# Kernel tuning notes

Hardware: AMD Instinct MI355X
Metric: run time of the kernel (lower is better)

Reference implementation:

```python
import jax, jax.numpy as jnp
import numpy as np

B, S, H, D = 2, 2048, 16, 64
DM = H * D  # 1024


def setup_inputs() -> dict:
    key = jax.random.key(0)
    ks = jax.random.split(key, 5)
    scale = 0.02
    return {
        "hidden_states": jax.random.normal(ks[0], (B, S, DM), dtype=jnp.float32),
        "Wq": scale * jax.random.normal(ks[1], (DM, DM), dtype=jnp.float32),
        "bq": jnp.zeros((DM,), jnp.float32),
        "Wk": scale * jax.random.normal(ks[2], (DM, DM), dtype=jnp.float32),
        "bk": jnp.zeros((DM,), jnp.float32),
        "Wv": scale * jax.random.normal(ks[3], (DM, DM), dtype=jnp.float32),
        "bv": jnp.zeros((DM,), jnp.float32),
        "Wy": scale * jax.random.normal(ks[4], (DM, DM), dtype=jnp.float32),
        "by": jnp.zeros((DM,), jnp.float32),
    }


def _split_heads(x):
    # [B,S,H*D] -> [B,H,S,D]
    b, s, _ = x.shape
    return x.reshape(b, s, H, D).transpose(0, 2, 1, 3)


def _merge_heads(x):
    # [B,H,S,D] -> [B,S,H*D]
    b, h, s, d = x.shape
    return x.transpose(0, 2, 1, 3).reshape(b, s, h * d)


def reference(hidden_states, Wq, bq, Wk, bk, Wv, bv, Wy, by):
    q = _split_heads(hidden_states @ Wq.T + bq)  # [B,H,S,D]
    k = _split_heads(hidden_states @ Wk.T + bk)
    v = _split_heads(hidden_states @ Wv.T + bv)

    logits = jnp.einsum("bhsd,bhtd->bhst", q, k) / jnp.sqrt(jnp.float32(D))
    mask = jnp.tril(jnp.ones((S, S), jnp.float32))  # causal lower-triangular mask

    # Faithful to the original module's hand-rolled masked softmax:
    # denominator = sum_t exp(logits) * mask ; numerator = exp(logits*mask - 1e4*(1-mask))
    denom = jnp.sum(jnp.exp(logits) * mask, axis=3, keepdims=True)
    numer = jnp.exp(logits * mask - 1e4 * (1.0 - mask))
    weights = numer / denom  # [B,H,S,S]

    attended = jnp.einsum("bhst,bhtd->bhsd", weights, v)
    out = _merge_heads(attended)  # [B,S,H*D]
    return out @ Wy.T + by
```

## Files before the change

kernel.cpp:

```cpp
#include <hip/hip_runtime.h>

#define DEV __device__ __forceinline__

typedef __attribute__((ext_vector_type(8))) short bf16x8;
typedef __attribute__((ext_vector_type(4))) float f32x4;
typedef __attribute__((ext_vector_type(16))) float f32x16;

DEV ushort f2bf(float f) {
  union { float f; unsigned u; } x; x.f = f;
  unsigned r = (x.u + 0x7FFFu + ((x.u >> 16) & 1u)) >> 16;
  return (ushort)r;
}

DEV void gload16(const void* g, void* l) {
  __builtin_amdgcn_global_load_lds(
      (const __attribute__((address_space(1))) void*)g,
      (__attribute__((address_space(3))) void*)l, 16, 0, 0);
}

DEV f32x4 mfma16(bf16x8 a, bf16x8 b, f32x4 c) {
  return __builtin_amdgcn_mfma_f32_16x16x32_bf16(a, b, c, 0, 0, 0);
}
DEV f32x16 mfma32(bf16x8 a, bf16x8 b, f32x16 c) {
  return __builtin_amdgcn_mfma_f32_32x32x16_bf16(a, b, c, 0, 0, 0);
}

DEV unsigned cvtpk(float a, float b) {
  unsigned r;
  asm("v_cvt_pk_bf16_f32 %0, %1, %2" : "=v"(r) : "v"(a), "v"(b));
  return r;
}

#if __has_builtin(__builtin_amdgcn_exp2f)
#define EXP2(x) __builtin_amdgcn_exp2f(x)
#else
#define EXP2(x) exp2f(x)
#endif

#define BB 2
#define SS 2048
#define HH 16
#define DD 64
#define DM 1024
#define MROWS (BB * SS)
#define NQKV  (3 * DM)
#define NQK   (2 * DM)

__global__ void convert_kernel(const float* __restrict__ hs,
                               const float* __restrict__ Wq, const float* __restrict__ bq,
                               const float* __restrict__ Wk, const float* __restrict__ bk,
                               const float* __restrict__ Wv, const float* __restrict__ bv,
                               const float* __restrict__ Wy,
                               ushort* __restrict__ Xb, ushort* __restrict__ Wqkv,
                               ushort* __restrict__ Wyb, float* __restrict__ bqkv) {
  const int HS_V = (MROWS * DM) / 4;
  const int WQ_V = (NQKV * DM) / 4;
  const int WY_V = (DM * DM) / 4;
  int idx = blockIdx.x * 256 + threadIdx.x;
  if (idx < HS_V) {
    float4 v = ((const float4*)hs)[idx];
    ushort4 o; o.x = f2bf(v.x); o.y = f2bf(v.y); o.z = f2bf(v.z); o.w = f2bf(v.w);
    ((ushort4*)Xb)[idx] = o;
  } else if (idx < HS_V + WQ_V) {
    int e = (idx - HS_V) * 4;
    int n = e >> 10, k = e & 1023;
    const float* W = (n < 1024) ? Wq : (n < 2048) ? Wk : Wv;
    int nn = n & 1023;
    float4 v = *(const float4*)(W + nn * 1024 + k);
    ushort4 o; o.x = f2bf(v.x); o.y = f2bf(v.y); o.z = f2bf(v.z); o.w = f2bf(v.w);
    ((ushort4*)Wqkv)[idx - HS_V] = o;
  } else if (idx < HS_V + WQ_V + WY_V) {
    int e = idx - HS_V - WQ_V;
    float4 v = ((const float4*)Wy)[e];
    ushort4 o; o.x = f2bf(v.x); o.y = f2bf(v.y); o.z = f2bf(v.z); o.w = f2bf(v.w);
    ((ushort4*)Wyb)[e] = o;
  }
  if (idx < NQKV)
    bqkv[idx] = (idx < 1024) ? bq[idx] : (idx < 2048) ? bk[idx - 1024] : bv[idx - 2048];
}

template <int BM, bool OUT_F32, bool VSPLIT>
__global__ void gemm_bt(const ushort* __restrict__ A, const ushort* __restrict__ Bw,
                        const float* __restrict__ bias, void* __restrict__ Cout,
                        ushort* __restrict__ VtOut,
                        int M, int N, int K, int Nc, int scaleN, float qscale) {
  constexpr int NI = BM / 32;
  __shared__ ushort Al[BM * 64];
  __shared__ ushort Bl[128 * 64];
  const int tid = threadIdx.x;
  const int lane = tid & 63;
  const int wave = tid >> 6;
  const int lg = lane >> 4, l15 = lane & 15;
  const int m0 = blockIdx.x * BM, n0 = blockIdx.y * 128;
  const int wm = (wave >> 1) * (BM / 2), wn = (wave & 1) * 64;

  f32x4 acc[NI][4] = {};

  for (int k0 = 0; k0 < K; k0 += 64) {
#pragma unroll
    for (int s = 0; s < BM * 8 / 256; ++s) {
      int f = tid + s * 256;
      int row = f >> 3, c = f & 7, cs = c ^ (row & 7);
      gload16(A + (size_t)(m0 + row) * K + k0 + cs * 8, (char*)Al + f * 16);
    }
#pragma unroll
    for (int s = 0; s < 4; ++s) {
      int f = tid + s * 256;
      int row = f >> 3, c = f & 7, cs = c ^ (row & 7);
      gload16(Bw + (size_t)(n0 + row) * K + k0 + cs * 8, (char*)Bl + f * 16);
    }
    __syncthreads();

#pragma unroll
    for (int kk = 0; kk < 2; ++kk) {
      bf16x8 af[NI], bfr[4];
#pragma unroll
      for (int i = 0; i < NI; ++i) {
        int rA = wm + i * 16 + l15;
        int cA = (kk * 4 + lg) ^ (rA & 7);
        af[i] = *(const bf16x8*)((const char*)Al + rA * 128 + cA * 16);
      }
#pragma unroll
      for (int j = 0; j < 4; ++j) {
        int rB = wn + j * 16 + l15;
        int cB = (kk * 4 + lg) ^ (rB & 7);
        bfr[j] = *(const bf16x8*)((const char*)Bl + rB * 128 + cB * 16);
      }
#pragma unroll
      for (int i = 0; i < NI; ++i)
#pragma unroll
        for (int j = 0; j < 4; ++j)
          acc[i][j] = mfma16(af[i], bfr[j], acc[i][j]);
    }
    __syncthreads();
  }

  if (VSPLIT && n0 >= 2048) {
#pragma unroll
    for (int i = 0; i < NI; ++i) {
#pragma unroll
      for (int j = 0; j < 4; ++j) {
        int n = n0 + wn + j * 16 + l15;
        float bv = bias[n];
        int h = (n >> 6) & 15, d = n & 63;
        int mb = m0 + wm + i * 16 + lg * 4;
        int b = mb >> 11, s = mb & 2047;
        ushort4 o;
        o.x = f2bf(acc[i][j][0] + bv);
        o.y = f2bf(acc[i][j][1] + bv);
        o.z = f2bf(acc[i][j][2] + bv);
        o.w = f2bf(acc[i][j][3] + bv);
        *(ushort4*)(VtOut + ((size_t)(b * 16 + h) * 64 + d) * SS + s) = o;
      }
    }
  } else {
#pragma unroll
    for (int i = 0; i < NI; ++i) {
#pragma unroll
      for (int j = 0; j < 4; ++j) {
        int n = n0 + wn + j * 16 + l15;
        float bv = bias[n];
        float qs = (n < scaleN) ? qscale : 1.0f;
#pragma unroll
        for (int r = 0; r < 4; ++r) {
          int m = m0 + wm + i * 16 + lg * 4 + r;
          float v = (acc[i][j][r] + bv) * qs;
          if (OUT_F32)
            ((float*)Cout)[(size_t)m * Nc + n] = v;
          else
            ((ushort*)Cout)[(size_t)m * Nc + n] = f2bf(v);
        }
      }
    }
  }
}

__global__ __launch_bounds__(256, 2)
void attn_kernel(const ushort* __restrict__ QK, const ushort* __restrict__ Vt,
                 ushort* __restrict__ Ob) {
  __shared__ __align__(16) char SMEM[65536];

  const int tid = threadIdx.x;
  const int wave = tid >> 6, lane = tid & 63;
  const int l31 = lane & 31, hi = lane >> 5;
  const int grp = wave >> 1, wq = wave & 1;

  const int n = blockIdx.x;
  const int bh = (n & 7) | ((n >> 7) << 3);
  const int pairi = (n >> 3) & 15;
  const int b = bh >> 4, h = bh & 15;

  int px = lane, pw = 1000;
  asm volatile("v_permlane32_swap_b32 %0, %1" : "+v"(px), "+v"(pw));
  const bool defA = (__builtin_amdgcn_readfirstlane(px) == 0);

  const int gtid = tid & 127;
  const int srow = gtid >> 3;
  const int scs = (gtid & 7) ^ (srow & 7);
  const ushort* Kg = QK + (size_t)(b * SS + srow) * NQK + DM + h * 64 + scs * 8;
  const ushort* Vg = Vt + (size_t)(bh * 64 + srow) * SS + scs * 8;

#define STAGE(d_, kv0_) do {                                            \
    const ushort* kg_ = Kg + (size_t)(kv0_) * NQK;                      \
    const ushort* vg_ = Vg + (kv0_);                                    \
    char* kl_ = SMEM + (grp * 2 + (d_)) * 8192 + gtid * 16;             \
    char* vl_ = SMEM + 32768 + (grp * 2 + (d_)) * 8192 + gtid * 16;     \
    _Pragma("unroll")                                                   \
    for (int s_ = 0; s_ < 4; ++s_) {                                    \
      gload16(kg_ + (size_t)s_ * 16 * NQK, kl_ + s_ * 2048);            \
      gload16(vg_ + (size_t)s_ * 16 * SS,  vl_ + s_ * 2048);            \
    }                                                                   \
  } while (0)

  union U4 { unsigned u[4]; bf16x8 v; };

#define PACKH(sv, R, D0, D1, D2, D3) do {                              \
    unsigned X = cvtpk(sv[R + 0], sv[R + 1]);                          \
    unsigned Y = cvtpk(sv[R + 2], sv[R + 3]);                          \
    unsigned W = cvtpk(sv[R + 4], sv[R + 5]);                          \
    unsigned Z = cvtpk(sv[R + 6], sv[R + 7]);                          \
    if (defA) {                                                        \
      asm volatile("v_permlane32_swap_b32 %0, %1" : "+v"(X), "+v"(W)); \
      asm volatile("v_permlane32_swap_b32 %0, %1" : "+v"(Y), "+v"(Z)); \
    } else {                                                           \
      asm volatile("v_permlane32_swap_b32 %0, %1" : "+v"(W), "+v"(X)); \
      asm volatile("v_permlane32_swap_b32 %0, %1" : "+v"(Z), "+v"(Y)); \
    }                                                                  \
    D0 = X; D1 = Y; D2 = W; D3 = Z;                                    \
  } while (0)

#pragma unroll 1
  for (int ph = 0; ph < 2; ++ph) {
    __builtin_amdgcn_s_barrier();

    const int qt = ph ? (31 - pairi) : pairi;
    const int q0 = qt * 64;
    const int nkv = qt + 1;
    const int niter = (nkv + 1) >> 1;
    const int qw = q0 + wq * 32;
    const int q_lane = qw + l31;

    const ushort* Qrow = QK + (size_t)(b * SS + q_lane) * NQK + h * 64 + hi * 8;
    bf16x8 qf0 = *(const bf16x8*)(Qrow);
    bf16x8 qf1 = *(const bf16x8*)(Qrow + 16);
    bf16x8 qf2 = *(const bf16x8*)(Qrow + 32);
    bf16x8 qf3 = *(const bf16x8*)(Qrow + 48);

    f32x16 acc0 = {}, acc1 = {};
    float ps0 = 0.f, ps1 = 0.f, ps2 = 0.f, ps3 = 0.f;

    if (grp < nkv) STAGE(0, grp * 64);
    int buf = 0;

#pragma unroll 1
    for (int it = 0; it < niter; ++it) {
      const int j = 2 * it + grp;
      if (j + 2 < nkv) {
        STAGE(buf ^ 1, (j + 2) * 64);
        asm volatile("s_waitcnt vmcnt(8)" ::: "memory");
      } else {
        asm volatile("s_waitcnt vmcnt(0)" ::: "memory");
      }
      __builtin_amdgcn_s_barrier();
      __builtin_amdgcn_sched_barrier(0);

      if (j < nkv) {
        const int kv0 = j * 64;
        const char* Kb = SMEM + (grp * 2 + buf) * 8192;
        const char* Vb = SMEM + 32768 + (grp * 2 + buf) * 8192;

        f32x16 s0 = {}, s1 = {};
        __builtin_amdgcn_s_setprio(1);
#pragma unroll
        for (int ks = 0; ks < 4; ++ks) {
          const int ch = (((ks * 2 + hi) ^ (l31 & 7)) * 16);
          bf16x8 kfa = *(const bf16x8*)(Kb + l31 * 128 + ch);
          bf16x8 kfb = *(const bf16x8*)(Kb + (l31 + 32) * 128 + ch);
          bf16x8 qk = (ks == 0) ? qf0 : (ks == 1) ? qf1 : (ks == 2) ? qf2 : qf3;
          s0 = mfma32(kfa, qk, s0);
          s1 = mfma32(kfb, qk, s1);
        }
        __builtin_amdgcn_s_setprio(0);

        if (j == qt) {
#pragma unroll
          for (int r = 0; r < 16; ++r) {
            const int tb = (r & 3) + 8 * (r >> 2) + 4 * hi;
            if (kv0 + tb > q_lane) s0[r] = -1e30f;
            if (kv0 + 32 + tb > q_lane) s1[r] = -1e30f;
          }
        }

#pragma unroll
        for (int r = 0; r < 16; r += 4) {
          float a0 = EXP2(s0[r]), a1 = EXP2(s0[r + 1]), a2 = EXP2(s0[r + 2]), a3 = EXP2(s0[r + 3]);
          s0[r] = a0; s0[r + 1] = a1; s0[r + 2] = a2; s0[r + 3] = a3;
          ps0 += a0; ps1 += a1; ps2 += a2; ps3 += a3;
          float b0 = EXP2(s1[r]), b1 = EXP2(s1[r + 1]), b2 = EXP2(s1[r + 2]), b3 = EXP2(s1[r + 3]);
          s1[r] = b0; s1[r + 1] = b1; s1[r + 2] = b2; s1[r + 3] = b3;
          ps0 += b0; ps1 += b1; ps2 += b2; ps3 += b3;
        }

        U4 f0, f1, f2, f3;
        PACKH(s0, 0, f0.u[0], f0.u[1], f0.u[2], f0.u[3]);
        PACKH(s0, 8, f1.u[0], f1.u[1], f1.u[2], f1.u[3]);
        PACKH(s1, 0, f2.u[0], f2.u[1], f2.u[2], f2.u[3]);
        PACKH(s1, 8, f3.u[0], f3.u[1], f3.u[2], f3.u[3]);

        __builtin_amdgcn_s_setprio(1);
#pragma unroll
        for (int ts = 0; ts < 4; ++ts) {
          const int ch = (((ts * 2 + hi) ^ (l31 & 7)) * 16);
          bf16x8 vfa = *(const bf16x8*)(Vb + l31 * 128 + ch);
          bf16x8 vfb = *(const bf16x8*)(Vb + (l31 + 32) * 128 + ch);
          bf16x8 pf = (ts == 0) ? f0.v : (ts == 1) ? f1.v : (ts == 2) ? f2.v : f3.v;
          acc0 = mfma32(vfa, pf, acc0);
          acc1 = mfma32(vfb, pf, acc1);
        }
        __builtin_amdgcn_s_setprio(0);
      }
      __builtin_amdgcn_sched_barrier(0);
      __builtin_amdgcn_s_barrier();
      buf ^= 1;
    }

    float psum = ps0 + ps1 + ps2 + ps3;
    f32x4* MA = (f32x4*)SMEM;
    float* MP = (float*)(SMEM + 32768);
    const int slot = wq * 64 + lane;
    if (grp == 1) {
#pragma unroll
      for (int c = 0; c < 4; ++c) {
        f32x4 t0 = {acc0[4 * c], acc0[4 * c + 1], acc0[4 * c + 2], acc0[4 * c + 3]};
        MA[c * 128 + slot] = t0;
        f32x4 t1 = {acc1[4 * c], acc1[4 * c + 1], acc1[4 * c + 2], acc1[4 * c + 3]};
        MA[(c + 4) * 128 + slot] = t1;
      }
      MP[slot] = psum;
    }
    __builtin_amdgcn_s_barrier();
    if (grp == 0) {
#pragma unroll
      for (int c = 0; c < 4; ++c) {
        f32x4 t0 = MA[c * 128 + slot];
        f32x4 t1 = MA[(c + 4) * 128 + slot];
        acc0[4 * c] += t0[0]; acc0[4 * c + 1] += t0[1];
        acc0[4 * c + 2] += t0[2]; acc0[4 * c + 3] += t0[3];
        acc1[4 * c] += t1[0]; acc1[4 * c + 1] += t1[1];
        acc1[4 * c + 2] += t1[2]; acc1[4 * c + 3] += t1[3];
      }
      psum += MP[slot];
      float tot = psum + __shfl_xor(psum, 32, 64);
      float inv = 1.0f / tot;
      ushort* orow = Ob + (size_t)(b * SS + q_lane) * DM + h * 64;
#pragma unroll
      for (int g = 0; g < 4; ++g) {
        uint2 st;
        st.x = cvtpk(acc0[4 * g + 0] * inv, acc0[4 * g + 1] * inv);
        st.y = cvtpk(acc0[4 * g + 2] * inv, acc0[4 * g + 3] * inv);
        *(uint2*)(orow + 8 * g + 4 * hi) = st;
        uint2 st2;
        st2.x = cvtpk(acc1[4 * g + 0] * inv, acc1[4 * g + 1] * inv);
        st2.y = cvtpk(acc1[4 * g + 2] * inv, acc1[4 * g + 3] * inv);
        *(uint2*)(orow + 32 + 8 * g + 4 * hi) = st2;
      }
    }
  }
#undef STAGE
#undef PACKH
}

extern "C" void kernel_launch(void* const* d_in, const int* in_sizes, int n_in,
                              void* d_out, int out_size, void* d_ws, size_t ws_size,
                              hipStream_t stream) {
  const float* hs = (const float*)d_in[0];
  const float* Wq = (const float*)d_in[1];
  const float* bq = (const float*)d_in[2];
  const float* Wk = (const float*)d_in[3];
  const float* bk = (const float*)d_in[4];
  const float* Wv = (const float*)d_in[5];
  const float* bv = (const float*)d_in[6];
  const float* Wy = (const float*)d_in[7];
  const float* by = (const float*)d_in[8];
  float* out = (float*)d_out;

  char* ws = (char*)d_ws;
  ushort* Xb   = (ushort*)(ws);
  ushort* Wqkv = (ushort*)(ws + (8ull  << 20));
  ushort* Wyb  = (ushort*)(ws + (14ull << 20));
  float*  bqkv = (float*) (ws + (16ull << 20));
  ushort* QK   = (ushort*)(ws + (17ull << 20));
  ushort* Vt   = (ushort*)(ws + (33ull << 20));
  ushort* Ob   = (ushort*)(ws + (41ull << 20));

  const float QSC = 0.125f * 1.44269504088896f;

  convert_kernel<<<dim3(8192), dim3(256), 0, stream>>>(hs, Wq, bq, Wk, bk, Wv, bv, Wy,
                                                       Xb, Wqkv, Wyb, bqkv);
  gemm_bt<128, false, true><<<dim3(32, 24), dim3(256), 0, stream>>>(
      Xb, Wqkv, bqkv, QK, Vt, MROWS, NQKV, DM, NQK, 1024, QSC);
  attn_kernel<<<dim3(512), dim3(256), 0, stream>>>(QK, Vt, Ob);
  gemm_bt<64, true, false><<<dim3(64, 8), dim3(256), 0, stream>>>(
      Ob, Wyb, by, out, nullptr, MROWS, DM, DM, DM, 0, 1.0f);
}
```

Baseline: 88.82 us.

## Double-buffer GEMM LDS tiles with async prefetch of next K-tile

```diff
diff --git a/kernel.cpp b/kernel.cpp
--- a/kernel.cpp
+++ b/kernel.cpp
@@ -80,13 +80,15 @@
 }
 
 template <int BM, bool OUT_F32, bool VSPLIT>
-__global__ void gemm_bt(const ushort* __restrict__ A, const ushort* __restrict__ Bw,
-                        const float* __restrict__ bias, void* __restrict__ Cout,
-                        ushort* __restrict__ VtOut,
-                        int M, int N, int K, int Nc, int scaleN, float qscale) {
+__global__ __launch_bounds__(256)
+void gemm_bt(const ushort* __restrict__ A, const ushort* __restrict__ Bw,
+             const float* __restrict__ bias, void* __restrict__ Cout,
+             ushort* __restrict__ VtOut,
+             int M, int N, int K, int Nc, int scaleN, float qscale) {
   constexpr int NI = BM / 32;
-  __shared__ ushort Al[BM * 64];
-  __shared__ ushort Bl[128 * 64];
+  constexpr int ASTEPS = BM / 32;
+  __shared__ ushort Al[2][BM * 64];
+  __shared__ ushort Bl[2][128 * 64];
   const int tid = threadIdx.x;
   const int lane = tid & 63;
   const int wave = tid >> 6;
@@ -96,20 +98,37 @@
 
   f32x4 acc[NI][4] = {};
 
-  for (int k0 = 0; k0 < K; k0 += 64) {
-#pragma unroll
-    for (int s = 0; s < BM * 8 / 256; ++s) {
-      int f = tid + s * 256;
-      int row = f >> 3, c = f & 7, cs = c ^ (row & 7);
-      gload16(A + (size_t)(m0 + row) * K + k0 + cs * 8, (char*)Al + f * 16);
-    }
-#pragma unroll
-    for (int s = 0; s < 4; ++s) {
-      int f = tid + s * 256;
-      int row = f >> 3, c = f & 7, cs = c ^ (row & 7);
-      gload16(Bw + (size_t)(n0 + row) * K + k0 + cs * 8, (char*)Bl + f * 16);
-    }
-    __syncthreads();
+  const int srow = tid >> 3;
+  const int scs = (tid & 7) ^ (srow & 7);
+
+#define STAGE(p_, k0_) do {                                               \
+    _Pragma("unroll")                                                     \
+    for (int s_ = 0; s_ < ASTEPS; ++s_)                                   \
+      gload16(A + (size_t)(m0 + srow + s_ * 32) * K + (k0_) + scs * 8,    \
+              (char*)Al[p_] + (tid + s_ * 256) * 16);                     \
+    _Pragma("unroll")                                                     \
+    for (int s_ = 0; s_ < 4; ++s_)                                        \
+      gload16(Bw + (size_t)(n0 + srow + s_ * 32) * K + (k0_) + scs * 8,   \
+              (char*)Bl[p_] + (tid + s_ * 256) * 16);                     \
+  } while (0)
+
+  const int nt = K >> 6;
+  int p = 0;
+  STAGE(0, 0);
+
+#pragma unroll 1
+  for (int t = 0; t < nt; ++t) {
+    if (t + 1 < nt) {
+      STAGE(p ^ 1, (t + 1) << 6);
+      if constexpr (ASTEPS + 4 == 8)
+        asm volatile("s_waitcnt vmcnt(8)" ::: "memory");
+      else
+        asm volatile("s_waitcnt vmcnt(6)" ::: "memory");
+    } else {
+      asm volatile("s_waitcnt vmcnt(0)" ::: "memory");
+    }
+    __builtin_amdgcn_s_barrier();
+    __builtin_amdgcn_sched_barrier(0);
 
 #pragma unroll
     for (int kk = 0; kk < 2; ++kk) {
@@ -118,13 +137,13 @@
       for (int i = 0; i < NI; ++i) {
         int rA = wm + i * 16 + l15;
         int cA = (kk * 4 + lg) ^ (rA & 7);
-        af[i] = *(const bf16x8*)((const char*)Al + rA * 128 + cA * 16);
+        af[i] = *(const bf16x8*)((const char*)Al[p] + rA * 128 + cA * 16);
       }
 #pragma unroll
       for (int j = 0; j < 4; ++j) {
         int rB = wn + j * 16 + l15;
         int cB = (kk * 4 + lg) ^ (rB & 7);
-        bfr[j] = *(const bf16x8*)((const char*)Bl + rB * 128 + cB * 16);
+        bfr[j] = *(const bf16x8*)((const char*)Bl[p] + rB * 128 + cB * 16);
       }
 #pragma unroll
       for (int i = 0; i < NI; ++i)
@@ -132,7 +151,9 @@
         for (int j = 0; j < 4; ++j)
           acc[i][j] = mfma16(af[i], bfr[j], acc[i][j]);
     }
-    __syncthreads();
+    __builtin_amdgcn_sched_barrier(0);
+    __builtin_amdgcn_s_barrier();
+    p ^= 1;
   }
 
   if (VSPLIT && n0 >= 2048) {
@@ -173,6 +194,7 @@
       }
     }
   }
+#undef STAGE
 }
 
 __global__ __launch_bounds__(256, 2)
```

New measurement: 100.5 us. 1.13x slower.
